# Kernel tuning notes

Measured on AMD Instinct MI355X. Metric: run time of the kernel, lower is better.

Reference implementation:

```python
import jax, jax.numpy as jnp
import numpy as np
import math

D_MODEL, D_K, D_V, N_HEADS = 1024, 64, 64, 16
B, LQ, LK = 4, 2048, 2048
LN_EPS = 1e-5


def setup_inputs() -> dict:
    key = jax.random.key(0)
    ks = jax.random.split(key, 8)
    s = 1.0 / math.sqrt(D_MODEL)
    return {
        "input_Q": jax.random.normal(ks[0], (B, LQ, D_MODEL), jnp.float32),
        "input_K": jax.random.normal(ks[1], (B, LK, D_MODEL), jnp.float32),
        "input_V": jax.random.normal(ks[2], (B, LK, D_MODEL), jnp.float32),
        "attn_mask": jax.random.randint(ks[3], (B, LQ, LK), 0, 2).astype(bool),
        # weights stored as [in, out] (torch Linear applies x @ W.T)
        "W_Q": jax.random.normal(ks[4], (D_MODEL, N_HEADS * D_K), jnp.float32) * s,
        "W_K": jax.random.normal(ks[5], (D_MODEL, N_HEADS * D_K), jnp.float32) * s,
        "W_V": jax.random.normal(ks[6], (D_MODEL, N_HEADS * D_V), jnp.float32) * s,
        "W_fc": jax.random.normal(ks[7], (N_HEADS * D_V, D_MODEL), jnp.float32) * s,
    }


def reference(input_Q, input_K, input_V, attn_mask, W_Q, W_K, W_V, W_fc):
    b, lq, _ = input_Q.shape
    lk = input_K.shape[1]
    # projections -> [b, len, h, d] -> [b, h, len, d]
    Q = (input_Q @ W_Q).reshape(b, lq, N_HEADS, D_K).transpose(0, 2, 1, 3)
    K = (input_K @ W_K).reshape(b, lk, N_HEADS, D_K).transpose(0, 2, 1, 3)
    V = (input_V @ W_V).reshape(b, lk, N_HEADS, D_V).transpose(0, 2, 1, 3)
    # scaled scores [b, h, q, k]
    scores = jnp.einsum("bhqd,bhkd->bhqk", Q, K) / math.sqrt(D_K)
    scores = jnp.where(attn_mask[:, None, :, :], -1e9, scores)
    attn = jax.nn.softmax(scores, axis=-1)
    # context [b, h, q, dv] -> [b, q, h*dv]
    ctx = jnp.einsum("bhqk,bhkd->bhqd", attn, V)
    ctx = ctx.transpose(0, 2, 1, 3).reshape(b, lq, N_HEADS * D_V)
    result = ctx @ W_fc
    x = result + input_Q
    mu = jnp.mean(x, axis=-1, keepdims=True)
    var = jnp.var(x, axis=-1, keepdims=True)
    res = (x - mu) / jnp.sqrt(var + LN_EPS)
    return res, attn
```

## Files before the change

kernel.cpp:

```cpp
#include <hip/hip_runtime.h>
#include <hip/hip_bf16.h>
#include <stdint.h>

#define DEVI __device__ __forceinline__

typedef __attribute__((ext_vector_type(8))) short bf16x8;
typedef __attribute__((ext_vector_type(4))) float f32x4;
typedef __attribute__((ext_vector_type(4))) unsigned u32x4;

static DEVI unsigned short f2bf(float f) {
  unsigned int u = __builtin_bit_cast(unsigned int, f);
  u = (u + 0x7FFFu + ((u >> 16) & 1u)) >> 16;
  return (unsigned short)u;
}

static DEVI void async16(const void* g, void* l) {
  __builtin_amdgcn_global_load_lds((__attribute__((address_space(1))) void*)(g),
                                   (__attribute__((address_space(3))) void*)(l),
                                   16, 0, 0);
}

__global__ __launch_bounds__(256) void cvt_kernel(const float* __restrict__ in,
                                                  unsigned short* __restrict__ out, int n4) {
  int i = blockIdx.x * 256 + threadIdx.x;
  if (i >= n4) return;
  float4 v = ((const float4*)in)[i];
  uint2 o;
  o.x = (unsigned)f2bf(v.x) | ((unsigned)f2bf(v.y) << 16);
  o.y = (unsigned)f2bf(v.z) | ((unsigned)f2bf(v.w) << 16);
  ((uint2*)out)[i] = o;
}

__global__ __launch_bounds__(256) void maskbits_kernel(const int* __restrict__ mask,
                                                       unsigned long long* __restrict__ mb) {
  size_t tg = (size_t)blockIdx.x * 256 + threadIdx.x;
  int v = mask[tg];
  unsigned long long bal = __ballot(v != 0);
  if ((threadIdx.x & 63) == 0) mb[tg >> 6] = bal;
}

__global__ __launch_bounds__(256) void wtrans_kernel(const float* __restrict__ W,
                                                     unsigned short* __restrict__ Wt,
                                                     float scale) {
  __shared__ float t[32][33];
  const int bx = blockIdx.x * 32;
  const int by = blockIdx.y * 32;
  const int tx = threadIdx.x, ty = threadIdx.y;
#pragma unroll
  for (int i = 0; i < 32; i += 8) t[ty + i][tx] = W[(size_t)(by + ty + i) * 1024 + bx + tx];
  __syncthreads();
#pragma unroll
  for (int i = 0; i < 32; i += 8)
    Wt[(size_t)(bx + ty + i) * 1024 + by + tx] = f2bf(t[tx][ty + i] * scale);
}

template <bool OUT_F32>
__global__ __launch_bounds__(256) void gemm_nt(const unsigned short* __restrict__ A, int lda,
                                               const unsigned short* __restrict__ B, int ldb,
                                               void* __restrict__ Cp, int ldc, int K) {
  __shared__ unsigned short As[128 * 64];
  __shared__ unsigned short Bs[128 * 64];
  const int tid = threadIdx.x;
  const int wave = tid >> 6, lane = tid & 63;
  const int m0 = blockIdx.x * 128, n0 = blockIdx.y * 128;
  const int wr = (wave >> 1) * 64, wc = (wave & 1) * 64;
  const int fr = lane & 15, fg = lane >> 4;
  f32x4 acc[4][4] = {};
  for (int kt = 0; kt < K; kt += 64) {
    __syncthreads();
#pragma unroll
    for (int it = 0; it < 4; ++it) {
      int id = it * 256 + tid;
      int row = id >> 3, ch = id & 7;
      async16(A + (size_t)(m0 + row) * lda + kt + ch * 8,
              (char*)As + (it * 256 + wave * 64) * 16);
      async16(B + (size_t)(n0 + row) * ldb + kt + ch * 8,
              (char*)Bs + (it * 256 + wave * 64) * 16);
    }
    __syncthreads();
#pragma unroll
    for (int ks = 0; ks < 2; ++ks) {
      bf16x8 af[4], bfr[4];
#pragma unroll
      for (int i = 0; i < 4; ++i)
        af[i] = *(const bf16x8*)(As + (wr + i * 16 + fr) * 64 + ks * 32 + fg * 8);
#pragma unroll
      for (int j = 0; j < 4; ++j)
        bfr[j] = *(const bf16x8*)(Bs + (wc + j * 16 + fr) * 64 + ks * 32 + fg * 8);
#pragma unroll
      for (int i = 0; i < 4; ++i)
#pragma unroll
        for (int j = 0; j < 4; ++j)
          acc[i][j] = __builtin_amdgcn_mfma_f32_16x16x32_bf16(af[i], bfr[j], acc[i][j], 0, 0, 0);
    }
  }
#pragma unroll
  for (int i = 0; i < 4; ++i)
#pragma unroll
    for (int j = 0; j < 4; ++j)
#pragma unroll
      for (int r = 0; r < 4; ++r) {
        int row = m0 + wr + i * 16 + fg * 4 + r;
        int col = n0 + wc + j * 16 + fr;
        if (OUT_F32)
          ((float*)Cp)[(size_t)row * ldc + col] = acc[i][j][r];
        else
          ((unsigned short*)Cp)[(size_t)row * ldc + col] = f2bf(acc[i][j][r]);
      }
}

__global__ __launch_bounds__(256) void vtrans_kernel(const unsigned short* __restrict__ Vp,
                                                     unsigned short* __restrict__ Vt) {
  __shared__ unsigned short t[64][72];
  const int bh = blockIdx.y;
  const int b = bh >> 4, h = bh & 15;
  const int l0 = blockIdx.x * 64;
  const int tid = threadIdx.x;
#pragma unroll
  for (int it = 0; it < 2; ++it) {
    int id = it * 256 + tid;
    int l = id >> 3, ch = id & 7;
    uint4 v = *(const uint4*)(Vp + (size_t)(b * 2048 + l0 + l) * 1024 + h * 64 + ch * 8);
    *(uint4*)(&t[l][ch * 8]) = v;
  }
  __syncthreads();
#pragma unroll
  for (int it = 0; it < 2; ++it) {
    int id = it * 256 + tid;
    int d = id >> 3, lc = id & 7;
    unsigned short o[8];
#pragma unroll
    for (int k = 0; k < 8; ++k) o[k] = t[lc * 8 + k][d];
    uint4 ov;
    ov.x = o[0] | ((unsigned)o[1] << 16);
    ov.y = o[2] | ((unsigned)o[3] << 16);
    ov.z = o[4] | ((unsigned)o[5] << 16);
    ov.w = o[6] | ((unsigned)o[7] << 16);
    *(uint4*)(Vt + ((size_t)bh * 64 + d) * 2048 + l0 + lc * 8) = ov;
  }
}

__global__ __launch_bounds__(512, 4) void attn_kernel(
    const unsigned short* __restrict__ Qp, const unsigned short* __restrict__ Kp,
    const unsigned short* __restrict__ Vt, const unsigned long long* __restrict__ mb,
    float* __restrict__ attn_out, unsigned short* __restrict__ ctx) {
  __shared__ unsigned short Ks[2][4096];
  __shared__ unsigned short Vs[2][4096];
  const int tid = threadIdx.x, wave = tid >> 6, lane = tid & 63;
  const int g = blockIdx.x;
  const int idx = g >> 3;
  const int bh = (g & 7) * 8 + (idx >> 4);
  const int b = bh >> 4, h = bh & 15;
  const int q0 = (idx & 15) * 128;
  const int fr = lane & 15, fg = lane >> 4;
  const int q = q0 + wave * 16 + fr;

  const int r0 = tid >> 3;
  const int chs = ((tid & 7) ^ (r0 & 7)) << 3;
  const unsigned short* kg = Kp + (size_t)(b * 2048 + r0) * 1024 + h * 64 + chs;
  const unsigned short* vg = Vt + (size_t)bh * 131072 + (size_t)r0 * 2048 + chs;

#define STAGE_K(buf, t) async16(kg + (size_t)(t) * 65536, (char*)Ks[buf] + wave * 1024)
#define STAGE_V(buf, t) async16(vg + (t) * 64, (char*)Vs[buf] + wave * 1024)

  const int c0 = (fg ^ (fr & 7)) << 3;
  const int c1 = ((4 + fg) ^ (fr & 7)) << 3;

  const unsigned short* qbase = Qp + (size_t)(b * 2048 + q) * 1024 + h * 64 + fg * 8;
  bf16x8 qa0 = *(const bf16x8*)(qbase);
  bf16x8 qa1 = *(const bf16x8*)(qbase + 32);

  const unsigned long long* mrow = mb + (size_t)(b * 2048 + q) * 32;
  const int msh = fg * 4;
  const float ninf = __uint_as_float(0xFF800000u);

  STAGE_K(0, 0);
  int cur = 0;
  float rsum = 0.f;
  for (int kt = 0; kt < 32; ++kt) {
    unsigned long long mw = mrow[kt];
    STAGE_K(cur ^ 1, (kt + 1) & 31);
    asm volatile("s_waitcnt vmcnt(2)" ::: "memory");
    __builtin_amdgcn_s_barrier();
    f32x4 s[4] = {};
#pragma unroll
    for (int j = 0; j < 4; ++j) {
      bf16x8 k0 = *(const bf16x8*)(&Ks[cur][(j * 16 + fr) * 64 + c0]);
      bf16x8 k1 = *(const bf16x8*)(&Ks[cur][(j * 16 + fr) * 64 + c1]);
      s[j] = __builtin_amdgcn_mfma_f32_16x16x32_bf16(k0, qa0, s[j], 0, 0, 0);
      s[j] = __builtin_amdgcn_mfma_f32_16x16x32_bf16(k1, qa1, s[j], 0, 0, 0);
    }
    unsigned mlo = (unsigned)mw, mhi = (unsigned)(mw >> 32);
#pragma unroll
    for (int j = 0; j < 4; ++j) {
      unsigned mj = ((j & 2) ? mhi : mlo) >> ((j & 1) * 16 + msh);
#pragma unroll
      for (int r = 0; r < 4; ++r) rsum += exp2f((mj & (1u << r)) ? ninf : s[j][r]);
    }
    asm volatile("s_waitcnt lgkmcnt(0)" ::: "memory");
    __builtin_amdgcn_s_barrier();
    cur ^= 1;
  }
  rsum += __shfl_xor(rsum, 16);
  rsum += __shfl_xor(rsum, 32);
  const float rs = 1.0f / rsum;

  STAGE_V(cur, 0);
  asm volatile("s_waitcnt vmcnt(0)" ::: "memory");
  __builtin_amdgcn_s_barrier();
  f32x4 o[4] = {};
  float* aout = attn_out + ((size_t)(bh * 2048 + q)) * 2048 + fg * 4;

  for (int kt = 0; kt < 32; ++kt) {
    unsigned long long mw = mrow[kt];
    STAGE_K(cur ^ 1, (kt + 1) & 31);
    STAGE_V(cur ^ 1, (kt + 1) & 31);
    asm volatile("s_waitcnt vmcnt(7)" ::: "memory");
    __builtin_amdgcn_s_barrier();
    f32x4 s[4] = {};
#pragma unroll
    for (int j = 0; j < 4; ++j) {
      bf16x8 k0 = *(const bf16x8*)(&Ks[cur][(j * 16 + fr) * 64 + c0]);
      bf16x8 k1 = *(const bf16x8*)(&Ks[cur][(j * 16 + fr) * 64 + c1]);
      s[j] = __builtin_amdgcn_mfma_f32_16x16x32_bf16(k0, qa0, s[j], 0, 0, 0);
      s[j] = __builtin_amdgcn_mfma_f32_16x16x32_bf16(k1, qa1, s[j], 0, 0, 0);
    }
    unsigned mlo = (unsigned)mw, mhi = (unsigned)(mw >> 32);
    unsigned pk[4][2];
#pragma unroll
    for (int j = 0; j < 4; ++j) {
      unsigned mj = ((j & 2) ? mhi : mlo) >> ((j & 1) * 16 + msh);
      float e0 = exp2f((mj & 1u) ? ninf : s[j][0]) * rs;
      float e1 = exp2f((mj & 2u) ? ninf : s[j][1]) * rs;
      float e2 = exp2f((mj & 4u) ? ninf : s[j][2]) * rs;
      float e3 = exp2f((mj & 8u) ? ninf : s[j][3]) * rs;
      f32x4 ev;
      ev[0] = e0; ev[1] = e1; ev[2] = e2; ev[3] = e3;
      __builtin_nontemporal_store(ev, (f32x4*)(aout + kt * 64 + j * 16));
      asm("v_cvt_pk_bf16_f32 %0, %1, %2" : "=v"(pk[j][0]) : "v"(e0), "v"(e1));
      asm("v_cvt_pk_bf16_f32 %0, %1, %2" : "=v"(pk[j][1]) : "v"(e2), "v"(e3));
    }
    unsigned x0 = pk[0][0], y0 = pk[1][0], x1 = pk[0][1], y1 = pk[1][1];
    unsigned x2 = pk[2][0], y2 = pk[3][0], x3 = pk[2][1], y3 = pk[3][1];
    asm("v_permlane32_swap_b32 %0, %1" : "+v"(x0), "+v"(y0));
    asm("v_permlane16_swap_b32 %0, %1" : "+v"(x0), "+v"(y0));
    asm("v_permlane32_swap_b32 %0, %1" : "+v"(x1), "+v"(y1));
    asm("v_permlane16_swap_b32 %0, %1" : "+v"(x1), "+v"(y1));
    asm("v_permlane32_swap_b32 %0, %1" : "+v"(x2), "+v"(y2));
    asm("v_permlane16_swap_b32 %0, %1" : "+v"(x2), "+v"(y2));
    asm("v_permlane32_swap_b32 %0, %1" : "+v"(x3), "+v"(y3));
    asm("v_permlane16_swap_b32 %0, %1" : "+v"(x3), "+v"(y3));
    u32x4 t0, t1;
    t0[0] = x0; t0[1] = x1; t0[2] = y0; t0[3] = y1;
    t1[0] = x2; t1[1] = x3; t1[2] = y2; t1[3] = y3;
    bf16x8 pa0 = __builtin_bit_cast(bf16x8, t0);
    bf16x8 pa1 = __builtin_bit_cast(bf16x8, t1);
#pragma unroll
    for (int ct = 0; ct < 4; ++ct) {
      bf16x8 v0 = *(const bf16x8*)(&Vs[cur][(ct * 16 + fr) * 64 + c0]);
      bf16x8 v1 = *(const bf16x8*)(&Vs[cur][(ct * 16 + fr) * 64 + c1]);
      o[ct] = __builtin_amdgcn_mfma_f32_16x16x32_bf16(pa0, v0, o[ct], 0, 0, 0);
      o[ct] = __builtin_amdgcn_mfma_f32_16x16x32_bf16(pa1, v1, o[ct], 0, 0, 0);
    }
    asm volatile("s_waitcnt lgkmcnt(0)" ::: "memory");
    __builtin_amdgcn_s_barrier();
    cur ^= 1;
  }
#pragma unroll
  for (int ct = 0; ct < 4; ++ct)
#pragma unroll
    for (int r = 0; r < 4; ++r)
      ctx[(size_t)(b * 2048 + q0 + wave * 16 + fg * 4 + r) * 1024 + h * 64 + ct * 16 + fr] =
          f2bf(o[ct][r]);
#undef STAGE_K
#undef STAGE_V
}

__global__ __launch_bounds__(256) void ln_kernel(const float* __restrict__ resl,
                                                 const float* __restrict__ inQ,
                                                 float* __restrict__ out) {
  __shared__ float red[8];
  const int row = blockIdx.x, tid = threadIdx.x;
  const int wave = tid >> 6, lane = tid & 63;
  float4 xv = ((const float4*)(resl + (size_t)row * 1024))[tid];
  float4 qv = ((const float4*)(inQ + (size_t)row * 1024))[tid];
  float v0 = xv.x + qv.x, v1 = xv.y + qv.y, v2 = xv.z + qv.z, v3 = xv.w + qv.w;
  float s = v0 + v1 + v2 + v3;
  float s2 = v0 * v0 + v1 * v1 + v2 * v2 + v3 * v3;
#pragma unroll
  for (int off = 1; off < 64; off <<= 1) {
    s += __shfl_xor(s, off);
    s2 += __shfl_xor(s2, off);
  }
  if (lane == 0) { red[wave] = s; red[4 + wave] = s2; }
  __syncthreads();
  s = red[0] + red[1] + red[2] + red[3];
  s2 = red[4] + red[5] + red[6] + red[7];
  const float mu = s * (1.0f / 1024.0f);
  const float var = s2 * (1.0f / 1024.0f) - mu * mu;
  const float inv = rsqrtf(var + 1e-5f);
  float4 ov;
  ov.x = (v0 - mu) * inv;
  ov.y = (v1 - mu) * inv;
  ov.z = (v2 - mu) * inv;
  ov.w = (v3 - mu) * inv;
  ((float4*)(out + (size_t)row * 1024))[tid] = ov;
}

extern "C" void kernel_launch(void* const* d_in, const int* in_sizes, int n_in, void* d_out,
                              int out_size, void* d_ws, size_t ws_size, hipStream_t stream) {
  const float* inQ = (const float*)d_in[0];
  const float* inK = (const float*)d_in[1];
  const float* inV = (const float*)d_in[2];
  const int* mask = (const int*)d_in[3];
  const float* WQ = (const float*)d_in[4];
  const float* WK = (const float*)d_in[5];
  const float* WV = (const float*)d_in[6];
  const float* WF = (const float*)d_in[7];
  float* res = (float*)d_out;
  float* attn = res + (size_t)8192 * 1024;

  char* w = (char*)d_ws;
  unsigned short* inQb = (unsigned short*)w; w += (size_t)16777216;
  unsigned short* inKb = (unsigned short*)w; w += (size_t)16777216;
  unsigned short* inVb = (unsigned short*)w; w += (size_t)16777216;
  unsigned short* WQt = (unsigned short*)w; w += (size_t)2097152;
  unsigned short* WKt = (unsigned short*)w; w += (size_t)2097152;
  unsigned short* WVt = (unsigned short*)w; w += (size_t)2097152;
  unsigned short* WFt = (unsigned short*)w; w += (size_t)2097152;
  unsigned short* Qp  = (unsigned short*)w; w += (size_t)16777216;
  unsigned short* Kp  = (unsigned short*)w; w += (size_t)16777216;
  unsigned short* Vp  = (unsigned short*)w; w += (size_t)16777216;
  unsigned short* Vtb = (unsigned short*)w; w += (size_t)16777216;
  unsigned short* ctx = (unsigned short*)w; w += (size_t)16777216;
  float* resl = (float*)w; w += (size_t)33554432;
  unsigned long long* mbits = (unsigned long long*)inQb;

  cvt_kernel<<<8192, 256, 0, stream>>>(inQ, inQb, 2097152);
  cvt_kernel<<<8192, 256, 0, stream>>>(inK, inKb, 2097152);
  cvt_kernel<<<8192, 256, 0, stream>>>(inV, inVb, 2097152);
  dim3 wb(32, 8);
  wtrans_kernel<<<dim3(32, 32), wb, 0, stream>>>(WQ, WQt, 0.18033688f);
  wtrans_kernel<<<dim3(32, 32), wb, 0, stream>>>(WK, WKt, 1.0f);
  wtrans_kernel<<<dim3(32, 32), wb, 0, stream>>>(WV, WVt, 1.0f);
  wtrans_kernel<<<dim3(32, 32), wb, 0, stream>>>(WF, WFt, 1.0f);
  gemm_nt<false><<<dim3(64, 8), 256, 0, stream>>>(inQb, 1024, WQt, 1024, Qp, 1024, 1024);
  gemm_nt<false><<<dim3(64, 8), 256, 0, stream>>>(inKb, 1024, WKt, 1024, Kp, 1024, 1024);
  gemm_nt<false><<<dim3(64, 8), 256, 0, stream>>>(inVb, 1024, WVt, 1024, Vp, 1024, 1024);
  maskbits_kernel<<<65536, 256, 0, stream>>>(mask, mbits);
  vtrans_kernel<<<dim3(32, 64), 256, 0, stream>>>(Vp, Vtb);
  attn_kernel<<<1024, 512, 0, stream>>>(Qp, Kp, Vtb, mbits, attn, ctx);
  gemm_nt<true><<<dim3(64, 8), 256, 0, stream>>>(ctx, 1024, WFt, 1024, resl, 1024, 1024);
  ln_kernel<<<8192, 256, 0, stream>>>(resl, inQ, res);
}
```

Baseline: 529.4 us.

## Triple-buffer K/V tiles with one barrier per iteration and prefetch mask words

Moves the attention kernel's K and V shared-memory staging from double to triple buffering. Prefetch now runs two tiles ahead, issued after a single barrier per iteration, which drops the trailing lgkmcnt wait and second barrier. Mask words are loaded one iteration ahead, and s_setprio raises wave priority around the MFMA blocks. In exchange, LDS use grows from 32KB to 48KB per block, which may cut occupancy at 4 blocks per CU, and the vmcnt counts must match the number of loads still in flight, including the nontemporal attn stores.

```diff
diff --git a/kernel.cpp b/kernel.cpp
--- a/kernel.cpp
+++ b/kernel.cpp
@@ -144,8 +144,8 @@
     const unsigned short* __restrict__ Qp, const unsigned short* __restrict__ Kp,
     const unsigned short* __restrict__ Vt, const unsigned long long* __restrict__ mb,
     float* __restrict__ attn_out, unsigned short* __restrict__ ctx) {
-  __shared__ unsigned short Ks[2][4096];
-  __shared__ unsigned short Vs[2][4096];
+  __shared__ unsigned short Ks[3][4096];
+  __shared__ unsigned short Vs[3][4096];
   const int tid = threadIdx.x, wave = tid >> 6, lane = tid & 63;
   const int g = blockIdx.x;
   const int idx = g >> 3;
@@ -175,57 +175,67 @@
   const float ninf = __uint_as_float(0xFF800000u);
 
   STAGE_K(0, 0);
-  int cur = 0;
+  STAGE_K(1, 1);
+  unsigned long long mw_cur = mrow[0];
   float rsum = 0.f;
+  int ri = 0, si = 2;
   for (int kt = 0; kt < 32; ++kt) {
-    unsigned long long mw = mrow[kt];
-    STAGE_K(cur ^ 1, (kt + 1) & 31);
-    asm volatile("s_waitcnt vmcnt(2)" ::: "memory");
+    unsigned long long mw_nxt = mrow[(kt + 1) & 31];
+    asm volatile("s_waitcnt vmcnt(3)" ::: "memory");
     __builtin_amdgcn_s_barrier();
+    STAGE_K(si, (kt + 2) & 31);
     f32x4 s[4] = {};
+    __builtin_amdgcn_s_setprio(1);
 #pragma unroll
     for (int j = 0; j < 4; ++j) {
-      bf16x8 k0 = *(const bf16x8*)(&Ks[cur][(j * 16 + fr) * 64 + c0]);
-      bf16x8 k1 = *(const bf16x8*)(&Ks[cur][(j * 16 + fr) * 64 + c1]);
+      bf16x8 k0 = *(const bf16x8*)(&Ks[ri][(j * 16 + fr) * 64 + c0]);
+      bf16x8 k1 = *(const bf16x8*)(&Ks[ri][(j * 16 + fr) * 64 + c1]);
       s[j] = __builtin_amdgcn_mfma_f32_16x16x32_bf16(k0, qa0, s[j], 0, 0, 0);
       s[j] = __builtin_amdgcn_mfma_f32_16x16x32_bf16(k1, qa1, s[j], 0, 0, 0);
     }
-    unsigned mlo = (unsigned)mw, mhi = (unsigned)(mw >> 32);
+    __builtin_amdgcn_s_setprio(0);
+    unsigned mlo = (unsigned)mw_cur, mhi = (unsigned)(mw_cur >> 32);
 #pragma unroll
     for (int j = 0; j < 4; ++j) {
       unsigned mj = ((j & 2) ? mhi : mlo) >> ((j & 1) * 16 + msh);
 #pragma unroll
       for (int r = 0; r < 4; ++r) rsum += exp2f((mj & (1u << r)) ? ninf : s[j][r]);
     }
-    asm volatile("s_waitcnt lgkmcnt(0)" ::: "memory");
-    __builtin_amdgcn_s_barrier();
-    cur ^= 1;
+    mw_cur = mw_nxt;
+    ri = (ri == 2) ? 0 : ri + 1;
+    si = (si == 2) ? 0 : si + 1;
   }
   rsum += __shfl_xor(rsum, 16);
   rsum += __shfl_xor(rsum, 32);
   const float rs = 1.0f / rsum;
 
-  STAGE_V(cur, 0);
+  STAGE_V(2, 0);
+  STAGE_V(0, 1);
+  mw_cur = mrow[0];
   asm volatile("s_waitcnt vmcnt(0)" ::: "memory");
   __builtin_amdgcn_s_barrier();
   f32x4 o[4] = {};
   float* aout = attn_out + ((size_t)(bh * 2048 + q)) * 2048 + fg * 4;
 
+  ri = 2;
+  si = 1;
   for (int kt = 0; kt < 32; ++kt) {
-    unsigned long long mw = mrow[kt];
-    STAGE_K(cur ^ 1, (kt + 1) & 31);
-    STAGE_V(cur ^ 1, (kt + 1) & 31);
-    asm volatile("s_waitcnt vmcnt(7)" ::: "memory");
+    unsigned long long mw_nxt = mrow[(kt + 1) & 31];
+    asm volatile("s_waitcnt vmcnt(12)" ::: "memory");
     __builtin_amdgcn_s_barrier();
+    STAGE_K(si, (kt + 2) & 31);
+    STAGE_V(si, (kt + 2) & 31);
     f32x4 s[4] = {};
+    __builtin_amdgcn_s_setprio(1);
 #pragma unroll
     for (int j = 0; j < 4; ++j) {
-      bf16x8 k0 = *(const bf16x8*)(&Ks[cur][(j * 16 + fr) * 64 + c0]);
-      bf16x8 k1 = *(const bf16x8*)(&Ks[cur][(j * 16 + fr) * 64 + c1]);
+      bf16x8 k0 = *(const bf16x8*)(&Ks[ri][(j * 16 + fr) * 64 + c0]);
+      bf16x8 k1 = *(const bf16x8*)(&Ks[ri][(j * 16 + fr) * 64 + c1]);
       s[j] = __builtin_amdgcn_mfma_f32_16x16x32_bf16(k0, qa0, s[j], 0, 0, 0);
       s[j] = __builtin_amdgcn_mfma_f32_16x16x32_bf16(k1, qa1, s[j], 0, 0, 0);
     }
-    unsigned mlo = (unsigned)mw, mhi = (unsigned)(mw >> 32);
+    __builtin_amdgcn_s_setprio(0);
+    unsigned mlo = (unsigned)mw_cur, mhi = (unsigned)(mw_cur >> 32);
     unsigned pk[4][2];
 #pragma unroll
     for (int j = 0; j < 4; ++j) {
@@ -255,16 +265,18 @@
     t1[0] = x2; t1[1] = x3; t1[2] = y2; t1[3] = y3;
     bf16x8 pa0 = __builtin_bit_cast(bf16x8, t0);
     bf16x8 pa1 = __builtin_bit_cast(bf16x8, t1);
+    __builtin_amdgcn_s_setprio(1);
 #pragma unroll
     for (int ct = 0; ct < 4; ++ct) {
-      bf16x8 v0 = *(const bf16x8*)(&Vs[cur][(ct * 16 + fr) * 64 + c0]);
-      bf16x8 v1 = *(const bf16x8*)(&Vs[cur][(ct * 16 + fr) * 64 + c1]);
+      bf16x8 v0 = *(const bf16x8*)(&Vs[ri][(ct * 16 + fr) * 64 + c0]);
+      bf16x8 v1 = *(const bf16x8*)(&Vs[ri][(ct * 16 + fr) * 64 + c1]);
       o[ct] = __builtin_amdgcn_mfma_f32_16x16x32_bf16(pa0, v0, o[ct], 0, 0, 0);
       o[ct] = __builtin_amdgcn_mfma_f32_16x16x32_bf16(pa1, v1, o[ct], 0, 0, 0);
     }
-    asm volatile("s_waitcnt lgkmcnt(0)" ::: "memory");
-    __builtin_amdgcn_s_barrier();
-    cur ^= 1;
+    __builtin_amdgcn_s_setprio(0);
+    mw_cur = mw_nxt;
+    ri = (ri == 2) ? 0 : ri + 1;
+    si = (si == 2) ? 0 : si + 1;
   }
 #pragma unroll
   for (int ct = 0; ct < 4; ++ct)
```

Result: slower. 565.2 us (+6.8%).
